# Kernel tuning notes

Measured on AMD Instinct MI355X. Metric: run time of the kernel, lower is better.

## Reference

```python
import jax, jax.numpy as jnp
import numpy as np

B, C, N, S = 4, 64, 16384, 16
DIM_OUT = 64
SCALE = DIM_OUT ** (-0.5)


def setup_inputs() -> dict:
    key = jax.random.key(0)
    ks = jax.random.split(key, 8)
    return {
        "xyz": jax.random.normal(ks[0], (B, 3, N), dtype=jnp.float32),
        "neighbor_xyz": jax.random.normal(ks[1], (B, 3, N, S), dtype=jnp.float32),
        "points": jax.random.normal(ks[2], (B, C, N), dtype=jnp.float32),
        "neighbor_points": jax.random.normal(ks[3], (B, C, N, S), dtype=jnp.float32),
        "Wk": jax.random.normal(ks[4], (C, C), dtype=jnp.float32) * 0.05,
        "Wv": jax.random.normal(ks[5], (DIM_OUT, C + 3), dtype=jnp.float32) * 0.05,
        "Wp": jax.random.normal(ks[6], (C, 4), dtype=jnp.float32) * 0.05,
        "bp": jax.random.normal(ks[7], (C,), dtype=jnp.float32) * 0.05,
    }


def reference(xyz, neighbor_xyz, points, neighbor_points, Wk, Wv, Wp, bp):
    # relative position of each neighbor: [B,3,N,S]
    tmp = xyz[:, :, :, None] - neighbor_xyz
    xyz_norm = jnp.sqrt(jnp.sum(tmp * tmp, axis=1, keepdims=True))  # [B,1,N,S]
    pos = jnp.concatenate([tmp, xyz_norm], axis=1)  # [B,4,N,S]

    # 1x1 convs == per-point channel matmuls
    pos_enc = jnp.einsum('oc,bcns->bons', Wp, pos) + bp[None, :, None, None]
    k = jnp.einsum('oc,bcns->bons', Wk, neighbor_points + pos_enc)  # [B,C,N,S]
    v_in = jnp.concatenate([neighbor_points, tmp], axis=1)  # [B,C+3,N,S]
    v = jnp.einsum('oc,bcns->bons', Wv, v_in)  # [B,dim_out,N,S]

    q = points * SCALE  # [B,C,N]
    attn = jax.nn.softmax(jnp.einsum('bcn,bcns->bns', q, k), axis=-1)  # [B,N,S]
    out = jnp.einsum('bns,bcns->bcn', attn, v)  # [B,dim_out,N]
    return out
```

## Files before the change

### kernel.cpp

```cpp
#include <hip/hip_runtime.h>
#include <math.h>

constexpr int Nn = 16384;
constexpr size_t NS = (size_t)Nn * 16;
constexpr int GPB = 4;

template <int CTRL>
__device__ __forceinline__ float dpp_f(float x) {
    return __int_as_float(
        __builtin_amdgcn_update_dpp(0, __float_as_int(x), CTRL, 0xF, 0xF, false));
}
__device__ __forceinline__ float qsum4(float v) {
    v += dpp_f<0xB1>(v);
    v += dpp_f<0x4E>(v);
    return v;
}
__device__ __forceinline__ float qmax4(float v) {
    v = fmaxf(v, dpp_f<0xB1>(v));
    v = fmaxf(v, dpp_f<0x4E>(v));
    return v;
}

#define BAR() do { asm volatile("s_waitcnt lgkmcnt(0)" ::: "memory"); \
    __builtin_amdgcn_s_barrier(); asm volatile("" ::: "memory"); } while (0)

__global__ __launch_bounds__(256, 3) void attn_fused_kernel(
    const float* __restrict__ xyz, const float* __restrict__ nxyz,
    const float* __restrict__ points, const float* __restrict__ npts,
    const float* __restrict__ Wk, const float* __restrict__ Wv,
    const float* __restrict__ Wp, float* __restrict__ out)
{
    __shared__ float wvT[67 * 68];
    __shared__ float qk_lds[64 * 68];
    __shared__ __align__(16) float lexch[4][64][4];
    __shared__ float vbexch[67 * 17];

    const int tid = threadIdx.x;
    const int w = tid >> 6;
    const int l = tid & 63;
    const int p = l >> 2;
    const int sq = l & 3;
    const int gptbase = blockIdx.x * (16 * GPB);
    const int b = gptbase >> 14;
    const int ngbase = gptbase & (Nn - 1);

    for (int idx = tid; idx < 64 * 67; idx += 256) {
        const int o = idx / 67, c = idx - o * 67;
        wvT[c * 68 + o] = Wv[idx];
    }

    const float* npb0 = npts + ((size_t)(b * 64 + 16 * w)) * NS + (size_t)ngbase * 16 + 4 * l;

    float4 npv4[16], nx[3];
    float xx[3] = {0, 0, 0};
    nx[0] = nx[1] = nx[2] = make_float4(0, 0, 0, 0);

    {
#pragma unroll
        for (int k = 0; k < 16; ++k) npv4[k] = *(const float4*)(npb0 + (size_t)k * NS);
        if (w == 3) {
            nx[0] = *(const float4*)(nxyz + ((size_t)(b * 3 + 0) * Nn + ngbase) * 16 + 4 * l);
            nx[1] = *(const float4*)(nxyz + ((size_t)(b * 3 + 1) * Nn + ngbase) * 16 + 4 * l);
            nx[2] = *(const float4*)(nxyz + ((size_t)(b * 3 + 2) * Nn + ngbase) * 16 + 4 * l);
            xx[0] = xyz[(size_t)(b * 3 + 0) * Nn + ngbase + p];
            xx[1] = xyz[(size_t)(b * 3 + 1) * Nn + ngbase + p];
            xx[2] = xyz[(size_t)(b * 3 + 2) * Nn + ngbase + p];
        }
    }

    {
        const int quarter = l >> 4;
        const int ptl = w * 16 + (l & 15);
        const int n = ngbase + ptl;

        float qk[16];
#pragma unroll
        for (int k = 0; k < 16; ++k) qk[k] = 0.f;

        const float* prow = points + (size_t)b * 64 * Nn + n;
        const float* wkq = Wk + 16 * quarter;
#pragma unroll 4
        for (int c = 0; c < 64; ++c) {
            const float qv = prow[(size_t)c * Nn];
            const float4 w0 = *(const float4*)(wkq + c * 64 + 0);
            const float4 w1 = *(const float4*)(wkq + c * 64 + 4);
            const float4 w2 = *(const float4*)(wkq + c * 64 + 8);
            const float4 w3 = *(const float4*)(wkq + c * 64 + 12);
            qk[0]  = fmaf(qv, w0.x, qk[0]);  qk[1]  = fmaf(qv, w0.y, qk[1]);
            qk[2]  = fmaf(qv, w0.z, qk[2]);  qk[3]  = fmaf(qv, w0.w, qk[3]);
            qk[4]  = fmaf(qv, w1.x, qk[4]);  qk[5]  = fmaf(qv, w1.y, qk[5]);
            qk[6]  = fmaf(qv, w1.z, qk[6]);  qk[7]  = fmaf(qv, w1.w, qk[7]);
            qk[8]  = fmaf(qv, w2.x, qk[8]);  qk[9]  = fmaf(qv, w2.y, qk[9]);
            qk[10] = fmaf(qv, w2.z, qk[10]); qk[11] = fmaf(qv, w2.w, qk[11]);
            qk[12] = fmaf(qv, w3.x, qk[12]); qk[13] = fmaf(qv, w3.y, qk[13]);
            qk[14] = fmaf(qv, w3.z, qk[14]); qk[15] = fmaf(qv, w3.w, qk[15]);
        }
#pragma unroll
        for (int k = 0; k < 16; ++k) qk[k] *= 0.125f;

        float p0 = 0.f, p1 = 0.f, p2 = 0.f, p3 = 0.f;
#pragma unroll
        for (int k = 0; k < 16; ++k) {
            const float4 wp4 = *(const float4*)(Wp + (16 * quarter + k) * 4);
            p0 = fmaf(qk[k], wp4.x, p0);
            p1 = fmaf(qk[k], wp4.y, p1);
            p2 = fmaf(qk[k], wp4.z, p2);
            p3 = fmaf(qk[k], wp4.w, p3);
        }
        p0 += __shfl_xor(p0, 16); p0 += __shfl_xor(p0, 32);
        p1 += __shfl_xor(p1, 16); p1 += __shfl_xor(p1, 32);
        p2 += __shfl_xor(p2, 16); p2 += __shfl_xor(p2, 32);
        p3 += __shfl_xor(p3, 16); p3 += __shfl_xor(p3, 32);

        float* orow = qk_lds + ptl * 68 + 16 * quarter;
        ((float4*)orow)[0] = make_float4(qk[0],  qk[1],  qk[2],  qk[3]);
        ((float4*)orow)[1] = make_float4(qk[4],  qk[5],  qk[6],  qk[7]);
        ((float4*)orow)[2] = make_float4(qk[8],  qk[9],  qk[10], qk[11]);
        ((float4*)orow)[3] = make_float4(qk[12], qk[13], qk[14], qk[15]);
        if (quarter == 0)
            *(float4*)(qk_lds + ptl * 68 + 64) = make_float4(p0, p1, p2, p3);
    }
    BAR();

#pragma unroll
    for (int g = 0; g < GPB; ++g) {
        const int ng = ngbase + 16 * g;

        const float* qrow = qk_lds + (16 * g + p) * 68 + 16 * w;
        const float4 qq0 = ((const float4*)qrow)[0];
        const float4 qq1 = ((const float4*)qrow)[1];
        const float4 qq2 = ((const float4*)qrow)[2];
        const float4 qq3 = ((const float4*)qrow)[3];
        float4 pp = make_float4(0, 0, 0, 0);

        float4 d04 = make_float4(0, 0, 0, 0), d14 = d04, d24 = d04, dn4 = d04;
        if (w == 3) {
            pp = *(const float4*)(qk_lds + (16 * g + p) * 68 + 64);
            d04 = make_float4(xx[0] - nx[0].x, xx[0] - nx[0].y, xx[0] - nx[0].z, xx[0] - nx[0].w);
            d14 = make_float4(xx[1] - nx[1].x, xx[1] - nx[1].y, xx[1] - nx[1].z, xx[1] - nx[1].w);
            d24 = make_float4(xx[2] - nx[2].x, xx[2] - nx[2].y, xx[2] - nx[2].z, xx[2] - nx[2].w);
            dn4 = make_float4(sqrtf(d04.x * d04.x + d14.x * d14.x + d24.x * d24.x),
                              sqrtf(d04.y * d04.y + d14.y * d14.y + d24.y * d24.y),
                              sqrtf(d04.z * d04.z + d14.z * d14.z + d24.z * d24.z),
                              sqrtf(d04.w * d04.w + d14.w * d14.w + d24.w * d24.w));
        }

        const float qks[16] = {qq0.x, qq0.y, qq0.z, qq0.w, qq1.x, qq1.y, qq1.z, qq1.w,
                               qq2.x, qq2.y, qq2.z, qq2.w, qq3.x, qq3.y, qq3.z, qq3.w};
        float4 lp = make_float4(0.f, 0.f, 0.f, 0.f);
#pragma unroll
        for (int k = 0; k < 16; ++k) {
            lp.x = fmaf(qks[k], npv4[k].x, lp.x);
            lp.y = fmaf(qks[k], npv4[k].y, lp.y);
            lp.z = fmaf(qks[k], npv4[k].z, lp.z);
            lp.w = fmaf(qks[k], npv4[k].w, lp.w);
        }
        if (w == 3) {
            lp.x += pp.x * d04.x + pp.y * d14.x + pp.z * d24.x + pp.w * dn4.x;
            lp.y += pp.x * d04.y + pp.y * d14.y + pp.z * d24.y + pp.w * dn4.y;
            lp.z += pp.x * d04.z + pp.y * d14.z + pp.z * d24.z + pp.w * dn4.z;
            lp.w += pp.x * d04.w + pp.y * d14.w + pp.z * d24.w + pp.w * dn4.w;
        }

        BAR();
        *(float4*)&lexch[w][l][0] = lp;
        BAR();
        const float4 g0 = *(const float4*)&lexch[0][l][0];
        const float4 g1 = *(const float4*)&lexch[1][l][0];
        const float4 g2 = *(const float4*)&lexch[2][l][0];
        const float4 g3 = *(const float4*)&lexch[3][l][0];
        const float4 lg = make_float4(g0.x + g1.x + g2.x + g3.x,
                                      g0.y + g1.y + g2.y + g3.y,
                                      g0.z + g1.z + g2.z + g3.z,
                                      g0.w + g1.w + g2.w + g3.w);

        float mx = fmaxf(fmaxf(lg.x, lg.y), fmaxf(lg.z, lg.w));
        mx = qmax4(mx);
        const float e0 = __expf(lg.x - mx), e1 = __expf(lg.y - mx);
        const float e2 = __expf(lg.z - mx), e3 = __expf(lg.w - mx);
        const float se = qsum4((e0 + e1) + (e2 + e3));
        const float inv = 1.0f / se;
        const float at0 = e0 * inv, at1 = e1 * inv, at2 = e2 * inv, at3 = e3 * inv;

#pragma unroll
        for (int k = 0; k < 16; ++k) {
            float v = at0 * npv4[k].x + at1 * npv4[k].y + at2 * npv4[k].z + at3 * npv4[k].w;
            v = qsum4(v);
            if (sq == (k & 3)) vbexch[(16 * w + k) * 17 + p] = v;
        }
        if (w == 3) {
            const float t0 = qsum4(at0 * d04.x + at1 * d04.y + at2 * d04.z + at3 * d04.w);
            const float t1 = qsum4(at0 * d14.x + at1 * d14.y + at2 * d14.z + at3 * d14.w);
            const float t2 = qsum4(at0 * d24.x + at1 * d24.y + at2 * d24.z + at3 * d24.w);
            if (sq == 0) vbexch[64 * 17 + p] = t0;
            else if (sq == 1) vbexch[65 * 17 + p] = t1;
            else if (sq == 2) vbexch[66 * 17 + p] = t2;
        }

        if (g + 1 < GPB) {
            const float* npb = npb0 + (size_t)(g + 1) * 256;
#pragma unroll
            for (int k = 0; k < 16; ++k) npv4[k] = *(const float4*)(npb + (size_t)k * NS);
            if (w == 3) {
                const int ng2 = ngbase + 16 * (g + 1);
                nx[0] = *(const float4*)(nxyz + ((size_t)(b * 3 + 0) * Nn + ng2) * 16 + 4 * l);
                nx[1] = *(const float4*)(nxyz + ((size_t)(b * 3 + 1) * Nn + ng2) * 16 + 4 * l);
                nx[2] = *(const float4*)(nxyz + ((size_t)(b * 3 + 2) * Nn + ng2) * 16 + 4 * l);
                xx[0] = xyz[(size_t)(b * 3 + 0) * Nn + ng2 + p];
                xx[1] = xyz[(size_t)(b * 3 + 1) * Nn + ng2 + p];
                xx[2] = xyz[(size_t)(b * 3 + 2) * Nn + ng2 + p];
            }
        }

        BAR();

        float4 oa = make_float4(0.f, 0.f, 0.f, 0.f);
#pragma unroll
        for (int c = 0; c < 67; ++c) {
            const float vb = vbexch[c * 17 + p];
            const float4 wq = *(const float4*)&wvT[c * 68 + 16 * w + 4 * sq];
            oa.x = fmaf(vb, wq.x, oa.x);
            oa.y = fmaf(vb, wq.y, oa.y);
            oa.z = fmaf(vb, wq.z, oa.z);
            oa.w = fmaf(vb, wq.w, oa.w);
        }

        float* ob = out + ((size_t)(b * 64 + 16 * w + 4 * sq)) * Nn + ng + p;
        ob[0]              = oa.x;
        ob[(size_t)Nn]     = oa.y;
        ob[(size_t)Nn * 2] = oa.z;
        ob[(size_t)Nn * 3] = oa.w;
    }
}

extern "C" void kernel_launch(void* const* d_in, const int* in_sizes, int n_in,
                              void* d_out, int out_size, void* d_ws, size_t ws_size,
                              hipStream_t stream) {
    const float* xyz    = (const float*)d_in[0];
    const float* nxyz   = (const float*)d_in[1];
    const float* points = (const float*)d_in[2];
    const float* npts   = (const float*)d_in[3];
    const float* Wk     = (const float*)d_in[4];
    const float* Wv     = (const float*)d_in[5];
    const float* Wp     = (const float*)d_in[6];
    float* out = (float*)d_out;

    hipLaunchKernelGGL(attn_fused_kernel, dim3(1024), dim3(256), 0, stream,
                       xyz, nxyz, points, npts, Wk, Wv, Wp, out);
}
```

Measured before the change: 119.2 us.

## Halve groups per block, store Wv as packed bf16 in LDS

Each block now handles 32 points instead of 64, and the launch grid doubles to 2048 blocks. The per-block q·Wk precompute is re-split so each lane covers 8 key channels, with an extra shuffle step. Wv is stored in LDS as packed bf16 pairs, which shrinks LDS use to allow more resident blocks and halves LDS reads in the output projection. The cost is bf16 rounding of Wv, which adds numerical error, and the per-block Wv staging now runs twice as often in total.

After: 300.4 us. 2.52x slower.

```diff
diff --git a/kernel.cpp b/kernel.cpp
--- a/kernel.cpp
+++ b/kernel.cpp
@@ -3,7 +3,7 @@
 
 constexpr int Nn = 16384;
 constexpr size_t NS = (size_t)Nn * 16;
-constexpr int GPB = 4;
+constexpr int GPB = 2;
 
 template <int CTRL>
 __device__ __forceinline__ float dpp_f(float x) {
@@ -20,6 +20,12 @@
     v = fmaxf(v, dpp_f<0x4E>(v));
     return v;
 }
+
+__device__ __forceinline__ unsigned bf16_rne(unsigned u) {
+    return (u + 0x7FFFu + ((u >> 16) & 1u)) >> 16;
+}
+__device__ __forceinline__ float blo(unsigned u) { return __uint_as_float(u << 16); }
+__device__ __forceinline__ float bhi(unsigned u) { return __uint_as_float(u & 0xFFFF0000u); }
 
 #define BAR() do { asm volatile("s_waitcnt lgkmcnt(0)" ::: "memory"); \
     __builtin_amdgcn_s_barrier(); asm volatile("" ::: "memory"); } while (0)
@@ -30,8 +36,8 @@
     const float* __restrict__ Wk, const float* __restrict__ Wv,
     const float* __restrict__ Wp, float* __restrict__ out)
 {
-    __shared__ float wvT[67 * 68];
-    __shared__ float qk_lds[64 * 68];
+    __shared__ __align__(16) unsigned wvP[34 * 68];
+    __shared__ __align__(16) float qk_lds[32 * 68];
     __shared__ __align__(16) float lexch[4][64][4];
     __shared__ float vbexch[67 * 17];
 
@@ -44,80 +50,71 @@
     const int b = gptbase >> 14;
     const int ngbase = gptbase & (Nn - 1);
 
-    for (int idx = tid; idx < 64 * 67; idx += 256) {
-        const int o = idx / 67, c = idx - o * 67;
-        wvT[c * 68 + o] = Wv[idx];
-    }
-
-    const float* npb0 = npts + ((size_t)(b * 64 + 16 * w)) * NS + (size_t)ngbase * 16 + 4 * l;
-
+    for (int i = tid; i < 64 * 34; i += 256) {
+        const int o = i / 34, cp = i - o * 34;
+        const int c0 = 2 * cp;
+        const unsigned ulo = __float_as_uint(Wv[o * 67 + c0]);
+        const unsigned uhi = (c0 + 1 < 67) ? __float_as_uint(Wv[o * 67 + c0 + 1]) : 0u;
+        wvP[cp * 68 + o] = bf16_rne(ulo) | (bf16_rne(uhi) << 16);
+    }
+
+    const float* npb0 = npts + (size_t)(b * 64 + 16 * w) * NS + (size_t)ngbase * 16 + 4 * l;
     float4 npv4[16], nx[3];
     float xx[3] = {0, 0, 0};
     nx[0] = nx[1] = nx[2] = make_float4(0, 0, 0, 0);
+#pragma unroll
+    for (int k = 0; k < 16; ++k) npv4[k] = *(const float4*)(npb0 + (size_t)k * NS);
+    if (w == 3) {
+        nx[0] = *(const float4*)(nxyz + ((size_t)(b * 3 + 0) * Nn + ngbase) * 16 + 4 * l);
+        nx[1] = *(const float4*)(nxyz + ((size_t)(b * 3 + 1) * Nn + ngbase) * 16 + 4 * l);
+        nx[2] = *(const float4*)(nxyz + ((size_t)(b * 3 + 2) * Nn + ngbase) * 16 + 4 * l);
+        xx[0] = xyz[(size_t)(b * 3 + 0) * Nn + ngbase + p];
+        xx[1] = xyz[(size_t)(b * 3 + 1) * Nn + ngbase + p];
+        xx[2] = xyz[(size_t)(b * 3 + 2) * Nn + ngbase + p];
+    }
 
     {
-#pragma unroll
-        for (int k = 0; k < 16; ++k) npv4[k] = *(const float4*)(npb0 + (size_t)k * NS);
-        if (w == 3) {
-            nx[0] = *(const float4*)(nxyz + ((size_t)(b * 3 + 0) * Nn + ngbase) * 16 + 4 * l);
-            nx[1] = *(const float4*)(nxyz + ((size_t)(b * 3 + 1) * Nn + ngbase) * 16 + 4 * l);
-            nx[2] = *(const float4*)(nxyz + ((size_t)(b * 3 + 2) * Nn + ngbase) * 16 + 4 * l);
-            xx[0] = xyz[(size_t)(b * 3 + 0) * Nn + ngbase + p];
-            xx[1] = xyz[(size_t)(b * 3 + 1) * Nn + ngbase + p];
-            xx[2] = xyz[(size_t)(b * 3 + 2) * Nn + ngbase + p];
-        }
-    }
-
-    {
-        const int quarter = l >> 4;
-        const int ptl = w * 16 + (l & 15);
+        const int e = l >> 3;
+        const int ptl = w * 8 + (l & 7);
         const int n = ngbase + ptl;
 
-        float qk[16];
-#pragma unroll
-        for (int k = 0; k < 16; ++k) qk[k] = 0.f;
+        float qk[8];
+#pragma unroll
+        for (int k = 0; k < 8; ++k) qk[k] = 0.f;
 
         const float* prow = points + (size_t)b * 64 * Nn + n;
-        const float* wkq = Wk + 16 * quarter;
+        const float* wkq = Wk + 8 * e;
 #pragma unroll 4
         for (int c = 0; c < 64; ++c) {
             const float qv = prow[(size_t)c * Nn];
             const float4 w0 = *(const float4*)(wkq + c * 64 + 0);
             const float4 w1 = *(const float4*)(wkq + c * 64 + 4);
-            const float4 w2 = *(const float4*)(wkq + c * 64 + 8);
-            const float4 w3 = *(const float4*)(wkq + c * 64 + 12);
-            qk[0]  = fmaf(qv, w0.x, qk[0]);  qk[1]  = fmaf(qv, w0.y, qk[1]);
-            qk[2]  = fmaf(qv, w0.z, qk[2]);  qk[3]  = fmaf(qv, w0.w, qk[3]);
-            qk[4]  = fmaf(qv, w1.x, qk[4]);  qk[5]  = fmaf(qv, w1.y, qk[5]);
-            qk[6]  = fmaf(qv, w1.z, qk[6]);  qk[7]  = fmaf(qv, w1.w, qk[7]);
-            qk[8]  = fmaf(qv, w2.x, qk[8]);  qk[9]  = fmaf(qv, w2.y, qk[9]);
-            qk[10] = fmaf(qv, w2.z, qk[10]); qk[11] = fmaf(qv, w2.w, qk[11]);
-            qk[12] = fmaf(qv, w3.x, qk[12]); qk[13] = fmaf(qv, w3.y, qk[13]);
-            qk[14] = fmaf(qv, w3.z, qk[14]); qk[15] = fmaf(qv, w3.w, qk[15]);
-        }
-#pragma unroll
-        for (int k = 0; k < 16; ++k) qk[k] *= 0.125f;
+            qk[0] = fmaf(qv, w0.x, qk[0]);  qk[1] = fmaf(qv, w0.y, qk[1]);
+            qk[2] = fmaf(qv, w0.z, qk[2]);  qk[3] = fmaf(qv, w0.w, qk[3]);
+            qk[4] = fmaf(qv, w1.x, qk[4]);  qk[5] = fmaf(qv, w1.y, qk[5]);
+            qk[6] = fmaf(qv, w1.z, qk[6]);  qk[7] = fmaf(qv, w1.w, qk[7]);
+        }
+#pragma unroll
+        for (int k = 0; k < 8; ++k) qk[k] *= 0.125f;
 
         float p0 = 0.f, p1 = 0.f, p2 = 0.f, p3 = 0.f;
 #pragma unroll
-        for (int k = 0; k < 16; ++k) {
-            const float4 wp4 = *(const float4*)(Wp + (16 * quarter + k) * 4);
+        for (int k = 0; k < 8; ++k) {
+            const float4 wp4 = *(const float4*)(Wp + (8 * e + k) * 4);
             p0 = fmaf(qk[k], wp4.x, p0);
             p1 = fmaf(qk[k], wp4.y, p1);
             p2 = fmaf(qk[k], wp4.z, p2);
             p3 = fmaf(qk[k], wp4.w, p3);
         }
-        p0 += __shfl_xor(p0, 16); p0 += __shfl_xor(p0, 32);
-        p1 += __shfl_xor(p1, 16); p1 += __shfl_xor(p1, 32);
-        p2 += __shfl_xor(p2, 16); p2 += __shfl_xor(p2, 32);
-        p3 += __shfl_xor(p3, 16); p3 += __shfl_xor(p3, 32);
-
-        float* orow = qk_lds + ptl * 68 + 16 * quarter;
-        ((float4*)orow)[0] = make_float4(qk[0],  qk[1],  qk[2],  qk[3]);
-        ((float4*)orow)[1] = make_float4(qk[4],  qk[5],  qk[6],  qk[7]);
-        ((float4*)orow)[2] = make_float4(qk[8],  qk[9],  qk[10], qk[11]);
-        ((float4*)orow)[3] = make_float4(qk[12], qk[13], qk[14], qk[15]);
-        if (quarter == 0)
+        p0 += __shfl_xor(p0, 8); p0 += __shfl_xor(p0, 16); p0 += __shfl_xor(p0, 32);
+        p1 += __shfl_xor(p1, 8); p1 += __shfl_xor(p1, 16); p1 += __shfl_xor(p1, 32);
+        p2 += __shfl_xor(p2, 8); p2 += __shfl_xor(p2, 16); p2 += __shfl_xor(p2, 32);
+        p3 += __shfl_xor(p3, 8); p3 += __shfl_xor(p3, 16); p3 += __shfl_xor(p3, 32);
+
+        float* orow = qk_lds + ptl * 68 + 8 * e;
+        ((float4*)orow)[0] = make_float4(qk[0], qk[1], qk[2], qk[3]);
+        ((float4*)orow)[1] = make_float4(qk[4], qk[5], qk[6], qk[7]);
+        if (e == 0)
             *(float4*)(qk_lds + ptl * 68 + 64) = make_float4(p0, p1, p2, p3);
     }
     BAR();
@@ -216,13 +213,14 @@
 
         float4 oa = make_float4(0.f, 0.f, 0.f, 0.f);
 #pragma unroll
-        for (int c = 0; c < 67; ++c) {
-            const float vb = vbexch[c * 17 + p];
-            const float4 wq = *(const float4*)&wvT[c * 68 + 16 * w + 4 * sq];
-            oa.x = fmaf(vb, wq.x, oa.x);
-            oa.y = fmaf(vb, wq.y, oa.y);
-            oa.z = fmaf(vb, wq.z, oa.z);
-            oa.w = fmaf(vb, wq.w, oa.w);
+        for (int cp = 0; cp < 34; ++cp) {
+            const float vb0 = vbexch[(2 * cp) * 17 + p];
+            const float vb1 = (2 * cp + 1 < 67) ? vbexch[(2 * cp + 1) * 17 + p] : 0.f;
+            const uint4 wq = *(const uint4*)&wvP[cp * 68 + 16 * w + 4 * sq];
+            oa.x = fmaf(vb0, blo(wq.x), oa.x); oa.x = fmaf(vb1, bhi(wq.x), oa.x);
+            oa.y = fmaf(vb0, blo(wq.y), oa.y); oa.y = fmaf(vb1, bhi(wq.y), oa.y);
+            oa.z = fmaf(vb0, blo(wq.z), oa.z); oa.z = fmaf(vb1, bhi(wq.z), oa.z);
+            oa.w = fmaf(vb0, blo(wq.w), oa.w); oa.w = fmaf(vb1, bhi(wq.w), oa.w);
         }
 
         float* ob = out + ((size_t)(b * 64 + 16 * w + 4 * sq)) * Nn + ng + p;
@@ -245,6 +243,6 @@
     const float* Wp     = (const float*)d_in[6];
     float* out = (float*)d_out;
 
-    hipLaunchKernelGGL(attn_fused_kernel, dim3(1024), dim3(256), 0, stream,
+    hipLaunchKernelGGL(attn_fused_kernel, dim3(2048), dim3(256), 0, stream,
                        xyz, nxyz, points, npts, Wk, Wv, Wp, out);
 }
```
